# Performance work log

Measured on AMD Instinct MI355X. Metric: run time of the kernel, lower is better.

## Reference

```python
import jax, jax.numpy as jnp
import numpy as np
from jax import lax

B, V, C, D, H, W = 1, 5, 32, 48, 128, 160
RATIO = 8


def setup_inputs() -> dict:
    key = jax.random.key(0)
    k1, k2, k3 = jax.random.split(key, 3)
    features = jax.random.normal(k1, (V, B, C, H, W), jnp.float32)
    # proj_matrices[b, v, 0] = 4x4 extrinsic, proj_matrices[b, v, 1, :3, :3] = intrinsic K
    f = 200.0
    K = np.array([[f, 0.0, W / 2.0], [0.0, f, H / 2.0], [0.0, 0.0, 1.0]], np.float32)
    proj = np.zeros((B, V, 2, 4, 4), np.float32)
    for v in range(V):
        E = np.eye(4, dtype=np.float32)
        E[0, 3] = 2.0 * v  # horizontal baseline per source view
        proj[:, v, 0] = E
        P1 = np.eye(4, dtype=np.float32)
        P1[:3, :3] = K
        proj[:, v, 1] = P1
    proj_matrices = jnp.asarray(proj)
    depth_values = jnp.broadcast_to(jnp.linspace(425.0, 935.0, D, dtype=jnp.float32), (B, D))
    mask = jax.random.normal(k2, (B, 9 * RATIO * RATIO, H, W), jnp.float32)
    W_reg = jax.random.normal(k3, (1, C, 3, 3, 3), jnp.float32) * 0.05
    return {"features": features, "proj_matrices": proj_matrices,
            "depth_values": depth_values, "mask": mask, "W_reg": W_reg}


def _combine(p):
    # p: [B,2,4,4] -> K @ E[:3,:4] written into top 3 rows of extrinsic (as in source)
    top = jnp.einsum('bij,bjk->bik', p[:, 1, :3, :3], p[:, 0, :3, :4])
    return p[:, 0].at[:, :3, :4].set(top)


def _bilinear_sample(src, x, y):
    # src [B,C,H,W]; x,y [B,P] pixel coords; zeros padding, align_corners=True
    Bs, Cs, Hs, Ws = src.shape
    x0 = jnp.floor(x)
    y0 = jnp.floor(y)
    wx = x - x0
    wy = y - y0
    src_flat = src.reshape(Bs, Cs, Hs * Ws)

    def gather(xi, yi, w):
        valid = (xi >= 0) & (xi <= Ws - 1) & (yi >= 0) & (yi <= Hs - 1)
        xi_c = jnp.clip(xi, 0, Ws - 1).astype(jnp.int32)
        yi_c = jnp.clip(yi, 0, Hs - 1).astype(jnp.int32)
        idx = (yi_c * Ws + xi_c)[:, None, :]
        vals = jnp.take_along_axis(src_flat, jnp.broadcast_to(idx, (Bs, Cs, idx.shape[-1])), axis=2)
        return vals * (w * valid)[:, None, :]

    return (gather(x0, y0, (1 - wx) * (1 - wy)) + gather(x0 + 1, y0, wx * (1 - wy))
            + gather(x0, y0 + 1, (1 - wx) * wy) + gather(x0 + 1, y0 + 1, wx * wy))


def _homo_warp(src_fea, src_proj, ref_proj, depth_values):
    # faithful homo_warping2: project ref pixel grid at each depth hypothesis into src view
    Bs, Cs, Hs, Ws = src_fea.shape
    Dd = depth_values.shape[1]
    proj = jnp.einsum('bij,bjk->bik', src_proj, jnp.linalg.inv(ref_proj))
    rot = proj[:, :3, :3]
    trans = proj[:, :3, 3]
    ys, xs = jnp.meshgrid(jnp.arange(Hs, dtype=src_fea.dtype), jnp.arange(Ws, dtype=src_fea.dtype), indexing='ij')
    xyz = jnp.stack([xs.ravel(), ys.ravel(), jnp.ones(Hs * Ws, dtype=src_fea.dtype)])  # [3,HW]
    rot_xyz = jnp.einsum('bij,jp->bip', rot, xyz)  # [B,3,HW]
    pts = rot_xyz[:, :, None, :] * depth_values[:, None, :, None] + trans[:, :, None, None]  # [B,3,D,HW]
    gx = pts[:, 0] / pts[:, 2]
    gy = pts[:, 1] / pts[:, 2]
    warped = _bilinear_sample(src_fea, gx.reshape(Bs, -1), gy.reshape(Bs, -1))
    return warped.reshape(Bs, Cs, Dd, Hs, Ws)


def _convex_upsample(depth, mask, r):
    # depth [N,1,H,W], mask [N,9*r*r,H,W] -> [N, r*H, r*W]
    N, _, Hh, Ww = depth.shape
    m = jax.nn.softmax(mask.reshape(N, 1, 9, r, r, Hh, Ww), axis=2)
    dp = jnp.pad(depth, ((0, 0), (0, 0), (1, 1), (1, 1)))
    nb = jnp.stack([dp[:, :, dy:dy + Hh, dx:dx + Ww] for dy in range(3) for dx in range(3)], axis=2)
    up = jnp.sum(m * nb[:, :, :, None, None], axis=2)  # [N,1,r,r,H,W]
    up = up.transpose(0, 1, 4, 2, 5, 3)  # [N,1,H,r,W,r]
    return up.reshape(N, r * Hh, r * Ww)


def reference(features, proj_matrices, depth_values, mask, W_reg):
    num_views = features.shape[0]
    Dd = depth_values.shape[1]
    ref_proj = _combine(proj_matrices[:, 0])
    # variance cost-volume accumulation over views (ref volume broadcast along D)
    vsum = features[0][:, :, None, :, :]
    vsq = vsum ** 2
    for v in range(1, num_views):
        src_proj = _combine(proj_matrices[:, v])
        wv = _homo_warp(features[v], src_proj, ref_proj, depth_values)
        vsum = vsum + wv
        vsq = vsq + wv * wv
    variance = vsq / num_views - (vsum / num_views) ** 2  # [B,C,D,H,W]
    # cost regularization stand-in: 3x3x3 conv C->1, SAME padding
    pre = lax.conv_general_dilated(variance, W_reg, (1, 1, 1), 'SAME',
                                   dimension_numbers=('NCDHW', 'OIDHW', 'NCDHW'))[:, 0]
    prob = jax.nn.softmax(pre, axis=1)  # [B,D,H,W]
    depth = jnp.sum(prob * depth_values[:, :, None, None], axis=1)  # [B,H,W]
    # photometric confidence (no-grad path): sliding sum of 4 along D, pad (1,2)
    pd = jnp.pad(prob, ((0, 0), (1, 2), (0, 0), (0, 0)))
    sum4 = pd[:, 0:Dd] + pd[:, 1:Dd + 1] + pd[:, 2:Dd + 2] + pd[:, 3:Dd + 3]
    di = jnp.sum(prob * jnp.arange(Dd, dtype=prob.dtype)[None, :, None, None], axis=1).astype(jnp.int32)
    di = jnp.clip(di, 0, Dd - 1)
    conf = jax.lax.stop_gradient(jnp.take_along_axis(sum4, di[:, None], axis=1)[:, 0])
    depth_up = _convex_upsample(depth[:, None], mask, RATIO)
    return (depth_up, depth, conf)
```

## Files before the change

### kernel.cpp

```cpp
#include <hip/hip_runtime.h>
#include <hip/hip_bf16.h>


#define NV 5
#define NC 32
#define ND 48
#define NH 128
#define NW 160
#define HW (NH * NW)
#define DHW (ND * HW)

typedef __attribute__((ext_vector_type(2))) float f32x2;
typedef __attribute__((ext_vector_type(2), aligned(4))) float f32x2u;

#define OFF_M      0
#define OFF_WF     256
#define OFF_DEPTHF 4096
#define OFF_PRE    86016
#define OFF_WV     4018176

__global__ void k_setup(const float* __restrict__ proj,
                        const float* __restrict__ wreg,
                        float* __restrict__ M, float* __restrict__ wf) {
  if (threadIdx.x != 0) return;
  double P[NV][2][4][4];
  for (int v = 0; v < NV; ++v)
    for (int m = 0; m < 2; ++m)
      for (int i = 0; i < 4; ++i)
        for (int j = 0; j < 4; ++j)
          P[v][m][i][j] = (double)proj[((v * 2 + m) * 4 + i) * 4 + j];
  double C[NV][4][4];
  for (int v = 0; v < NV; ++v) {
    for (int i = 0; i < 4; ++i)
      for (int j = 0; j < 4; ++j) C[v][i][j] = P[v][0][i][j];
    for (int i = 0; i < 3; ++i)
      for (int j = 0; j < 4; ++j) {
        double s = 0.0;
        for (int k = 0; k < 3; ++k) s += P[v][1][i][k] * P[v][0][k][j];
        C[v][i][j] = s;
      }
  }
  double a[4][8];
  for (int i = 0; i < 4; ++i)
    for (int j = 0; j < 4; ++j) { a[i][j] = C[0][i][j]; a[i][j + 4] = (i == j) ? 1.0 : 0.0; }
  for (int col = 0; col < 4; ++col) {
    int piv = col; double best = fabs(a[col][col]);
    for (int r = col + 1; r < 4; ++r) { double v = fabs(a[r][col]); if (v > best) { best = v; piv = r; } }
    if (piv != col)
      for (int j = 0; j < 8; ++j) { double t = a[col][j]; a[col][j] = a[piv][j]; a[piv][j] = t; }
    double pv = a[col][col];
    for (int j = 0; j < 8; ++j) a[col][j] /= pv;
    for (int r = 0; r < 4; ++r) if (r != col) {
      double f = a[r][col];
      for (int j = 0; j < 8; ++j) a[r][j] -= f * a[col][j];
    }
  }
  double inv[4][4];
  for (int i = 0; i < 4; ++i)
    for (int j = 0; j < 4; ++j) inv[i][j] = a[i][j + 4];
  for (int v = 1; v < NV; ++v) {
    float* m = M + (v - 1) * 12;
    for (int i = 0; i < 3; ++i) {
      double r[4] = {0, 0, 0, 0};
      for (int k = 0; k < 4; ++k) {
        double cv = C[v][i][k];
        for (int j = 0; j < 4; ++j) r[j] += cv * inv[k][j];
      }
      m[i * 3 + 0] = (float)r[0]; m[i * 3 + 1] = (float)r[1]; m[i * 3 + 2] = (float)r[2];
      m[9 + i] = (float)r[3];
    }
  }
  for (int c = 0; c < NC; ++c) {
    for (int t = 0; t < 27; ++t) wf[c * 28 + t] = wreg[c * 27 + t];
    wf[c * 28 + 27] = 0.f;
  }
}

__global__ __launch_bounds__(256) void k_warpvar(
    const float* __restrict__ feat,
    const float* __restrict__ depthv,
    const float* __restrict__ M,
    const float* __restrict__ wf,
    __hip_bfloat16* __restrict__ WV)
{
  int idx = blockIdx.x * 256 + threadIdx.x;
  int x = idx % NW;
  int t1 = idx / NW;
  int y = t1 % NH;
  int d = t1 / NH;
  float xf = (float)x, yf = (float)y;
  float df = depthv[d];

  int   r0i[4], r1i[4];
  float W00[4], W10[4], W01[4], W11[4];
#pragma unroll
  for (int v = 0; v < 4; ++v) {
    const float* m = M + v * 12;
    float rx = m[0] * xf + m[1] * yf + m[2];
    float ry = m[3] * xf + m[4] * yf + m[5];
    float rz = m[6] * xf + m[7] * yf + m[8];
    float px = rx * df + m[9];
    float py = ry * df + m[10];
    float pz = rz * df + m[11];
    float gx = px / pz;
    float gy = py / pz;
    float x0f = floorf(gx), y0f = floorf(gy);
    float wx = gx - x0f, wy = gy - y0f;
    float vx0 = (x0f >= 0.f && x0f <= (float)(NW - 1)) ? 1.f : 0.f;
    float vx1 = (x0f + 1.f >= 0.f && x0f + 1.f <= (float)(NW - 1)) ? 1.f : 0.f;
    float vy0 = (y0f >= 0.f && y0f <= (float)(NH - 1)) ? 1.f : 0.f;
    float vy1 = (y0f + 1.f >= 0.f && y0f + 1.f <= (float)(NH - 1)) ? 1.f : 0.f;
    float xbf = fminf(fmaxf(x0f, 0.f), (float)(NW - 2));
    int xb = (int)xbf;
    float wl = (1.f - wx) * vx0;
    float wr = wx * vx1;
    bool leftIsP1 = (x0f > (float)(NW - 2));
    bool rightIsP0 = (x0f < 0.f);
    float ax = (leftIsP1 ? 0.f : wl) + (rightIsP0 ? wr : 0.f);
    float bx = (leftIsP1 ? wl : 0.f) + (rightIsP0 ? 0.f : wr);
    float yb0f = fminf(fmaxf(y0f, 0.f), (float)(NH - 1));
    float yb1f = fminf(fmaxf(y0f + 1.f, 0.f), (float)(NH - 1));
    r0i[v] = (int)yb0f * NW + xb;
    r1i[v] = (int)yb1f * NW + xb;
    float wy0 = (1.f - wy) * vy0, wy1 = wy * vy1;
    W00[v] = ax * wy0; W10[v] = bx * wy0;
    W01[v] = ax * wy1; W11[v] = bx * wy1;
  }

  int pix = y * NW + x;
  f32x2 wv2[14];
#pragma unroll
  for (int u = 0; u < 14; ++u) wv2[u] = (f32x2){0.f, 0.f};

#pragma unroll
  for (int c = 0; c < NC; ++c) {
    float f0 = feat[c * HW + pix];
    float vs = f0, vq = f0 * f0;
#pragma unroll
    for (int v = 0; v < 4; ++v) {
      const float* fv = feat + ((size_t)((v + 1) * NC + c)) * HW;
      f32x2u q0 = *(const f32x2u*)(fv + r0i[v]);
      f32x2u q1 = *(const f32x2u*)(fv + r1i[v]);
      float val = W00[v] * q0.x + W10[v] * q0.y
                + W01[v] * q1.x + W11[v] * q1.y;
      vs += val;
      vq += val * val;
    }
    float var = vq * 0.2f - (vs * 0.2f) * (vs * 0.2f);
    const f32x2* wrow = (const f32x2*)(wf + c * 28);
    f32x2 vv; vv.x = var; vv.y = var;
#pragma unroll
    for (int u = 0; u < 14; ++u) wv2[u] += wrow[u] * vv;
  }

#pragma unroll
  for (int u = 0; u < 14; ++u) {
    int t0 = 2 * u;
    WV[(size_t)t0 * DHW + idx] = __float2bfloat16(wv2[u].x);
    if (t0 + 1 < 27) WV[(size_t)(t0 + 1) * DHW + idx] = __float2bfloat16(wv2[u].y);
  }
}

__global__ __launch_bounds__(256) void k_conv(const __hip_bfloat16* __restrict__ WV,
                                              float* __restrict__ pre) {
  int idx = blockIdx.x * 256 + threadIdx.x;
  int x = idx % NW;
  int t1 = idx / NW;
  int y = t1 % NH;
  int d = t1 / NH;
  float acc = 0.f;
#pragma unroll
  for (int dd = 0; dd < 3; ++dd) {
    int dp = d + dd - 1;
    bool dok = (dp >= 0) && (dp < ND);
    int dpc = min(max(dp, 0), ND - 1);
#pragma unroll
    for (int i = 0; i < 3; ++i) {
      int yp = y + i - 1;
      bool yok = (yp >= 0) && (yp < NH);
      int ypc = min(max(yp, 0), NH - 1);
#pragma unroll
      for (int j = 0; j < 3; ++j) {
        int xp = x + j - 1;
        bool xok = (xp >= 0) && (xp < NW);
        int xpc = min(max(xp, 0), NW - 1);
        int t = dd * 9 + i * 3 + j;
        float v = __bfloat162float(WV[(size_t)t * DHW + dpc * HW + ypc * NW + xpc]);
        acc += (dok && yok && xok) ? v : 0.f;
      }
    }
  }
  pre[idx] = acc;
}

__global__ __launch_bounds__(256) void k_softmax(const float* __restrict__ pre,
                                                 const float* __restrict__ depthv,
                                                 float* __restrict__ depthf,
                                                 float* __restrict__ out_depth,
                                                 float* __restrict__ out_conf) {
  int p = blockIdx.x * 256 + threadIdx.x;
  float pr[ND];
  float m = -1e30f;
#pragma unroll
  for (int d = 0; d < ND; ++d) { pr[d] = pre[d * HW + p]; m = fmaxf(m, pr[d]); }
  float s = 0.f;
#pragma unroll
  for (int d = 0; d < ND; ++d) { pr[d] = expf(pr[d] - m); s += pr[d]; }
  float inv = 1.f / s;
  float dep = 0.f, ti = 0.f;
#pragma unroll
  for (int d = 0; d < ND; ++d) {
    float prob = pr[d] * inv;
    pr[d] = prob;
    dep += prob * depthv[d];
    ti += prob * (float)d;
  }
  int di = (int)ti;
  di = di < 0 ? 0 : (di > ND - 1 ? ND - 1 : di);
  float conf = 0.f;
#pragma unroll
  for (int d = 0; d < ND; ++d)
    conf += (d >= di - 1 && d <= di + 2) ? pr[d] : 0.f;
  depthf[p] = dep;
  out_depth[p] = dep;
  out_conf[p] = conf;
}

__global__ __launch_bounds__(640) void k_upsample(const float* __restrict__ mask,
                                                  const float* __restrict__ depthf,
                                                  float* __restrict__ out) {
  __shared__ float row[NW * 8];
  int y = blockIdx.x >> 3;
  int dy = blockIdx.x & 7;
#pragma unroll
  for (int rep = 0; rep < 2; ++rep) {
    int lin = rep * 640 + threadIdx.x;
    int dx = lin / NW;
    int x = lin % NW;
    float mv[9];
    float mmax = -1e30f;
#pragma unroll
    for (int k = 0; k < 9; ++k) {
      mv[k] = mask[(size_t)(k * 64 + dy * 8 + dx) * HW + y * NW + x];
      mmax = fmaxf(mmax, mv[k]);
    }
    float s = 0.f;
#pragma unroll
    for (int k = 0; k < 9; ++k) { mv[k] = expf(mv[k] - mmax); s += mv[k]; }
    float acc = 0.f;
#pragma unroll
    for (int k = 0; k < 9; ++k) {
      int ky = y + k / 3 - 1;
      int kx = x + k % 3 - 1;
      bool ok = (ky >= 0) && (ky < NH) && (kx >= 0) && (kx < NW);
      int kyc = min(max(ky, 0), NH - 1);
      int kxc = min(max(kx, 0), NW - 1);
      float dv = depthf[kyc * NW + kxc];
      acc += mv[k] * (ok ? dv : 0.f);
    }
    row[x * 8 + dx] = acc / s;
  }
  __syncthreads();
  float* orow = out + (size_t)(y * 8 + dy) * (NW * 8);
#pragma unroll
  for (int rep = 0; rep < 2; ++rep) {
    int j = rep * 640 + threadIdx.x;
    orow[j] = row[j];
  }
}

extern "C" void kernel_launch(void* const* d_in, const int* in_sizes, int n_in,
                              void* d_out, int out_size, void* d_ws, size_t ws_size,
                              hipStream_t stream) {
  const float* feat   = (const float*)d_in[0];
  const float* proj   = (const float*)d_in[1];
  const float* depthv = (const float*)d_in[2];
  const float* mask   = (const float*)d_in[3];
  const float* wreg   = (const float*)d_in[4];

  char* ws = (char*)d_ws;
  float* M       = (float*)(ws + OFF_M);
  float* wf      = (float*)(ws + OFF_WF);
  float* depthf  = (float*)(ws + OFF_DEPTHF);
  float* pre     = (float*)(ws + OFF_PRE);
  __hip_bfloat16* WV = (__hip_bfloat16*)(ws + OFF_WV);

  float* out = (float*)d_out;
  float* out_depth = out + (NH * 8) * (NW * 8);
  float* out_conf  = out_depth + HW;

  k_setup<<<1, 64, 0, stream>>>(proj, wreg, M, wf);
  k_warpvar<<<DHW / 256, 256, 0, stream>>>(feat, depthv, M, wf, WV);
  k_conv<<<DHW / 256, 256, 0, stream>>>(WV, pre);
  k_softmax<<<HW / 256, 256, 0, stream>>>(pre, depthv, depthf, out_depth, out_conf);
  k_upsample<<<NH * 8, 640, 0, stream>>>(mask, depthf, out);
}
```

Before: 276.4 us.

## Add fast path for pure horizontal-shift homographies in warp-variance kernel

The setup kernel now checks whether each source-view homography reduces to identity plus an x-translation. If it does, it precomputes a per-view, per-depth integer shift and fractional weight table and sets a flag. When the flag is set, the warp-variance kernel skips the projective divide and the second row gather. That halves the feature loads per view and removes most of the per-pixel coordinate math. The general bilinear path stays as a fallback. The new table and flag share workspace offsets with the depth buffer, which works only because of the kernel execution order.

```diff
diff --git a/kernel.cpp b/kernel.cpp
--- a/kernel.cpp
+++ b/kernel.cpp
@@ -15,13 +15,17 @@
 
 #define OFF_M      0
 #define OFF_WF     256
+#define OFF_TBL    4096
+#define OFF_FLAG   5632
 #define OFF_DEPTHF 4096
 #define OFF_PRE    86016
 #define OFF_WV     4018176
 
 __global__ void k_setup(const float* __restrict__ proj,
                         const float* __restrict__ wreg,
-                        float* __restrict__ M, float* __restrict__ wf) {
+                        const float* __restrict__ depthv,
+                        float* __restrict__ M, float* __restrict__ wf,
+                        float* __restrict__ tbl, int* __restrict__ flag) {
   if (threadIdx.x != 0) return;
   double P[NV][2][4][4];
   for (int v = 0; v < NV; ++v)
@@ -58,7 +62,11 @@
   double inv[4][4];
   for (int i = 0; i < 4; ++i)
     for (int j = 0; j < 4; ++j) inv[i][j] = a[i][j + 4];
+
+  bool shiftOK = true;
+  double Tx[4];
   for (int v = 1; v < NV; ++v) {
+    double rm[12];
     float* m = M + (v - 1) * 12;
     for (int i = 0; i < 3; ++i) {
       double r[4] = {0, 0, 0, 0};
@@ -66,13 +74,42 @@
         double cv = C[v][i][k];
         for (int j = 0; j < 4; ++j) r[j] += cv * inv[k][j];
       }
+      rm[i * 3 + 0] = r[0]; rm[i * 3 + 1] = r[1]; rm[i * 3 + 2] = r[2];
+      rm[9 + i] = r[3];
       m[i * 3 + 0] = (float)r[0]; m[i * 3 + 1] = (float)r[1]; m[i * 3 + 2] = (float)r[2];
       m[9 + i] = (float)r[3];
     }
+    for (int i = 0; i < 3; ++i)
+      for (int j = 0; j < 3; ++j) {
+        double want = (i == j) ? 1.0 : 0.0;
+        if (fabs(rm[i * 3 + j] - want) > 1e-4) shiftOK = false;
+      }
+    if (fabs(rm[10]) > 1e-4 || fabs(rm[11]) > 1e-4) shiftOK = false;
+    Tx[v - 1] = rm[9];
+  }
+  *flag = shiftOK ? 1 : 0;
+  if (shiftOK) {
+    for (int v = 0; v < 4; ++v)
+      for (int d = 0; d < ND; ++d) {
+        double off = Tx[v] / (double)depthv[d];
+        double s = floor(off);
+        tbl[(v * ND + d) * 2 + 0] = (float)s;
+        tbl[(v * ND + d) * 2 + 1] = (float)(off - s);
+      }
   }
   for (int c = 0; c < NC; ++c) {
     for (int t = 0; t < 27; ++t) wf[c * 28 + t] = wreg[c * 27 + t];
     wf[c * 28 + 27] = 0.f;
+  }
+}
+
+__device__ __forceinline__ void warpvar_store(
+    const f32x2* wv2, __hip_bfloat16* __restrict__ WV, int idx) {
+#pragma unroll
+  for (int u = 0; u < 14; ++u) {
+    int t0 = 2 * u;
+    WV[(size_t)t0 * DHW + idx] = __float2bfloat16(wv2[u].x);
+    if (t0 + 1 < 27) WV[(size_t)(t0 + 1) * DHW + idx] = __float2bfloat16(wv2[u].y);
   }
 }
 
@@ -81,6 +118,8 @@
     const float* __restrict__ depthv,
     const float* __restrict__ M,
     const float* __restrict__ wf,
+    const float* __restrict__ tbl,
+    const int* __restrict__ flag,
     __hip_bfloat16* __restrict__ WV)
 {
   int idx = blockIdx.x * 256 + threadIdx.x;
@@ -88,77 +127,108 @@
   int t1 = idx / NW;
   int y = t1 % NH;
   int d = t1 / NH;
-  float xf = (float)x, yf = (float)y;
-  float df = depthv[d];
-
-  int   r0i[4], r1i[4];
-  float W00[4], W10[4], W01[4], W11[4];
-#pragma unroll
-  for (int v = 0; v < 4; ++v) {
-    const float* m = M + v * 12;
-    float rx = m[0] * xf + m[1] * yf + m[2];
-    float ry = m[3] * xf + m[4] * yf + m[5];
-    float rz = m[6] * xf + m[7] * yf + m[8];
-    float px = rx * df + m[9];
-    float py = ry * df + m[10];
-    float pz = rz * df + m[11];
-    float gx = px / pz;
-    float gy = py / pz;
-    float x0f = floorf(gx), y0f = floorf(gy);
-    float wx = gx - x0f, wy = gy - y0f;
-    float vx0 = (x0f >= 0.f && x0f <= (float)(NW - 1)) ? 1.f : 0.f;
-    float vx1 = (x0f + 1.f >= 0.f && x0f + 1.f <= (float)(NW - 1)) ? 1.f : 0.f;
-    float vy0 = (y0f >= 0.f && y0f <= (float)(NH - 1)) ? 1.f : 0.f;
-    float vy1 = (y0f + 1.f >= 0.f && y0f + 1.f <= (float)(NH - 1)) ? 1.f : 0.f;
-    float xbf = fminf(fmaxf(x0f, 0.f), (float)(NW - 2));
-    int xb = (int)xbf;
-    float wl = (1.f - wx) * vx0;
-    float wr = wx * vx1;
-    bool leftIsP1 = (x0f > (float)(NW - 2));
-    bool rightIsP0 = (x0f < 0.f);
-    float ax = (leftIsP1 ? 0.f : wl) + (rightIsP0 ? wr : 0.f);
-    float bx = (leftIsP1 ? wl : 0.f) + (rightIsP0 ? 0.f : wr);
-    float yb0f = fminf(fmaxf(y0f, 0.f), (float)(NH - 1));
-    float yb1f = fminf(fmaxf(y0f + 1.f, 0.f), (float)(NH - 1));
-    r0i[v] = (int)yb0f * NW + xb;
-    r1i[v] = (int)yb1f * NW + xb;
-    float wy0 = (1.f - wy) * vy0, wy1 = wy * vy1;
-    W00[v] = ax * wy0; W10[v] = bx * wy0;
-    W01[v] = ax * wy1; W11[v] = bx * wy1;
-  }
-
   int pix = y * NW + x;
+
   f32x2 wv2[14];
 #pragma unroll
   for (int u = 0; u < 14; ++u) wv2[u] = (f32x2){0.f, 0.f};
 
-#pragma unroll
-  for (int c = 0; c < NC; ++c) {
-    float f0 = feat[c * HW + pix];
-    float vs = f0, vq = f0 * f0;
+  if (*flag) {
+    int   xb[4];
+    float A[4], B[4];
 #pragma unroll
     for (int v = 0; v < 4; ++v) {
-      const float* fv = feat + ((size_t)((v + 1) * NC + c)) * HW;
-      f32x2u q0 = *(const f32x2u*)(fv + r0i[v]);
-      f32x2u q1 = *(const f32x2u*)(fv + r1i[v]);
-      float val = W00[v] * q0.x + W10[v] * q0.y
-                + W01[v] * q1.x + W11[v] * q1.y;
-      vs += val;
-      vq += val * val;
-    }
-    float var = vq * 0.2f - (vs * 0.2f) * (vs * 0.2f);
-    const f32x2* wrow = (const f32x2*)(wf + c * 28);
-    f32x2 vv; vv.x = var; vv.y = var;
-#pragma unroll
-    for (int u = 0; u < 14; ++u) wv2[u] += wrow[u] * vv;
-  }
-
-#pragma unroll
-  for (int u = 0; u < 14; ++u) {
-    int t0 = 2 * u;
-    WV[(size_t)t0 * DHW + idx] = __float2bfloat16(wv2[u].x);
-    if (t0 + 1 < 27) WV[(size_t)(t0 + 1) * DHW + idx] = __float2bfloat16(wv2[u].y);
-  }
+      float sf = tbl[(v * ND + d) * 2 + 0];
+      float w  = tbl[(v * ND + d) * 2 + 1];
+      int sx = (int)sf;
+      int x0 = x + sx;
+      float wl = (x0 >= 0 && x0 <= NW - 1) ? (1.f - w) : 0.f;
+      float wr = (x0 >= -1 && x0 <= NW - 2) ? w : 0.f;
+      bool leftIsP1 = (x0 >= NW - 1);
+      bool rightIsP0 = (x0 < 0);
+      A[v] = (leftIsP1 ? 0.f : wl) + (rightIsP0 ? wr : 0.f);
+      B[v] = (leftIsP1 ? wl : 0.f) + (rightIsP0 ? 0.f : wr);
+      int xc = min(max(x0, 0), NW - 2);
+      xb[v] = y * NW + xc;
+    }
+#pragma unroll
+    for (int c = 0; c < NC; ++c) {
+      float f0 = feat[c * HW + pix];
+      float vs = f0, vq = f0 * f0;
+#pragma unroll
+      for (int v = 0; v < 4; ++v) {
+        const float* fv = feat + ((size_t)((v + 1) * NC + c)) * HW;
+        f32x2u q = *(const f32x2u*)(fv + xb[v]);
+        float val = A[v] * q.x + B[v] * q.y;
+        vs += val;
+        vq += val * val;
+      }
+      float var = vq * 0.2f - (vs * 0.2f) * (vs * 0.2f);
+      const f32x2* wrow = (const f32x2*)(wf + c * 28);
+      f32x2 vv; vv.x = var; vv.y = var;
+#pragma unroll
+      for (int u = 0; u < 14; ++u) wv2[u] += wrow[u] * vv;
+    }
+  } else {
+    float xf = (float)x, yf = (float)y;
+    float df = depthv[d];
+    int   r0i[4], r1i[4];
+    float W00[4], W10[4], W01[4], W11[4];
+#pragma unroll
+    for (int v = 0; v < 4; ++v) {
+      const float* m = M + v * 12;
+      float rx = m[0] * xf + m[1] * yf + m[2];
+      float ry = m[3] * xf + m[4] * yf + m[5];
+      float rz = m[6] * xf + m[7] * yf + m[8];
+      float px = rx * df + m[9];
+      float py = ry * df + m[10];
+      float pz = rz * df + m[11];
+      float gx = px / pz;
+      float gy = py / pz;
+      float x0f = floorf(gx), y0f = floorf(gy);
+      float wx = gx - x0f, wy = gy - y0f;
+      float vx0 = (x0f >= 0.f && x0f <= (float)(NW - 1)) ? 1.f : 0.f;
+      float vx1 = (x0f + 1.f >= 0.f && x0f + 1.f <= (float)(NW - 1)) ? 1.f : 0.f;
+      float vy0 = (y0f >= 0.f && y0f <= (float)(NH - 1)) ? 1.f : 0.f;
+      float vy1 = (y0f + 1.f >= 0.f && y0f + 1.f <= (float)(NH - 1)) ? 1.f : 0.f;
+      float xbf = fminf(fmaxf(x0f, 0.f), (float)(NW - 2));
+      int xbv = (int)xbf;
+      float wl = (1.f - wx) * vx0;
+      float wr = wx * vx1;
+      bool leftIsP1 = (x0f > (float)(NW - 2));
+      bool rightIsP0 = (x0f < 0.f);
+      float ax = (leftIsP1 ? 0.f : wl) + (rightIsP0 ? wr : 0.f);
+      float bx = (leftIsP1 ? wl : 0.f) + (rightIsP0 ? 0.f : wr);
+      float yb0f = fminf(fmaxf(y0f, 0.f), (float)(NH - 1));
+      float yb1f = fminf(fmaxf(y0f + 1.f, 0.f), (float)(NH - 1));
+      r0i[v] = (int)yb0f * NW + xbv;
+      r1i[v] = (int)yb1f * NW + xbv;
+      float wy0 = (1.f - wy) * vy0, wy1 = wy * vy1;
+      W00[v] = ax * wy0; W10[v] = bx * wy0;
+      W01[v] = ax * wy1; W11[v] = bx * wy1;
+    }
+#pragma unroll
+    for (int c = 0; c < NC; ++c) {
+      float f0 = feat[c * HW + pix];
+      float vs = f0, vq = f0 * f0;
+#pragma unroll
+      for (int v = 0; v < 4; ++v) {
+        const float* fv = feat + ((size_t)((v + 1) * NC + c)) * HW;
+        f32x2u q0 = *(const f32x2u*)(fv + r0i[v]);
+        f32x2u q1 = *(const f32x2u*)(fv + r1i[v]);
+        float val = W00[v] * q0.x + W10[v] * q0.y
+                  + W01[v] * q1.x + W11[v] * q1.y;
+        vs += val;
+        vq += val * val;
+      }
+      float var = vq * 0.2f - (vs * 0.2f) * (vs * 0.2f);
+      const f32x2* wrow = (const f32x2*)(wf + c * 28);
+      f32x2 vv; vv.x = var; vv.y = var;
+#pragma unroll
+      for (int u = 0; u < 14; ++u) wv2[u] += wrow[u] * vv;
+    }
+  }
+  warpvar_store(wv2, WV, idx);
 }
 
 __global__ __launch_bounds__(256) void k_conv(const __hip_bfloat16* __restrict__ WV,
@@ -281,6 +351,8 @@
   char* ws = (char*)d_ws;
   float* M       = (float*)(ws + OFF_M);
   float* wf      = (float*)(ws + OFF_WF);
+  float* tbl     = (float*)(ws + OFF_TBL);
+  int*   flag    = (int*)(ws + OFF_FLAG);
   float* depthf  = (float*)(ws + OFF_DEPTHF);
   float* pre     = (float*)(ws + OFF_PRE);
   __hip_bfloat16* WV = (__hip_bfloat16*)(ws + OFF_WV);
@@ -289,8 +361,8 @@
   float* out_depth = out + (NH * 8) * (NW * 8);
   float* out_conf  = out_depth + HW;
 
-  k_setup<<<1, 64, 0, stream>>>(proj, wreg, M, wf);
-  k_warpvar<<<DHW / 256, 256, 0, stream>>>(feat, depthv, M, wf, WV);
+  k_setup<<<1, 64, 0, stream>>>(proj, wreg, depthv, M, wf, tbl, flag);
+  k_warpvar<<<DHW / 256, 256, 0, stream>>>(feat, depthv, M, wf, tbl, flag, WV);
   k_conv<<<DHW / 256, 256, 0, stream>>>(WV, pre);
   k_softmax<<<HW / 256, 256, 0, stream>>>(pre, depthv, depthf, out_depth, out_conf);
   k_upsample<<<NH * 8, 640, 0, stream>>>(mask, depthf, out);
```

After: 330.3 us. 1.19x slower.
